# Performance work log

Measured on AMD Instinct MI355X. Metric: run time of the kernel, lower is better.

Reference implementation:

```python
import jax, jax.numpy as jnp
import numpy as np

ORDER = 24
N_POINTS = 524288


def setup_inputs() -> dict:
    key = jax.random.key(0)
    k1, k2 = jax.random.split(key)
    xyz = jax.random.uniform(k1, (N_POINTS, 3), dtype=jnp.float32)
    coeffs = jax.random.normal(k2, (ORDER ** 3,), dtype=jnp.float32) * 0.1
    return {"xyz": xyz, "coeffs": coeffs}


def reference(xyz, coeffs):
    # Faithful to: sum_{i,j,k} c[i,j,k] * sin(2pi i x) * sin(2pi j y) * sin(2pi k z)
    # but with per-axis sin tables computed once (O(order) transcendentals per point)
    # and the triple sum expressed as chained contractions (GEMM-like).
    order = ORDER
    C = coeffs.reshape(order, order, order)  # c[i,j,k]
    n = jnp.arange(order, dtype=xyz.dtype)   # frequencies 0..order-1 (i=0 row is all zeros)
    two_pi = jnp.asarray(2.0 * np.pi, dtype=xyz.dtype)
    S = jnp.sin(two_pi * xyz[:, :, None] * n)  # [N, 3, order]
    Sx, Sy, Sz = S[:, 0, :], S[:, 1, :], S[:, 2, :]  # each [N, order]
    A = jnp.einsum('nk,ijk->nij', Sz, C)   # [N, order, order]
    B = jnp.einsum('nj,nij->ni', Sy, A)    # [N, order]
    return jnp.einsum('ni,ni->n', Sx, B)   # [N]
```

## Files before the change

kernel.cpp:

```cpp
#include <hip/hip_runtime.h>

typedef _Float16 f16x2 __attribute__((ext_vector_type(2)));
typedef _Float16 f16x8 __attribute__((ext_vector_type(8)));
typedef __fp16   fp16v2 __attribute__((ext_vector_type(2)));
typedef float    f32x4 __attribute__((ext_vector_type(4)));
typedef unsigned int u32x4 __attribute__((ext_vector_type(4)));

#define TSTRIDE 17

__device__ __forceinline__ f16x2 pk2(float lo, float hi) {
    fp16v2 p = __builtin_amdgcn_cvt_pkrtz(lo, hi);
    return __builtin_bit_cast(f16x2, p);
}

__global__ __launch_bounds__(256) void prep_B(const float* __restrict__ coeffs,
                                              f16x8* __restrict__ wsB)
{
    int chunk = blockIdx.x * 256 + threadIdx.x;
    int f  = chunk / 48, sl = chunk % 48;
    int s  = f >> 1,  tt = f & 1;
    int gg = sl >> 4, cc = sl & 15;
    int i  = 16 * tt + cc;
    f16x8 v;
    if (i < 24) {
        const float* src = coeffs + i * 576 + s * 24 + gg * 8;
#pragma unroll
        for (int e = 0; e < 8; ++e) v[e] = (_Float16)src[e];
    } else {
#pragma unroll
        for (int e = 0; e < 8; ++e) v[e] = (_Float16)0.f;
    }
    wsB[chunk] = v;
}

__global__ __launch_bounds__(512, 4) void fourier_main(
    const float* __restrict__ xyz,
    const f16x8* __restrict__ wsB,
    float* __restrict__ out)
{
    __shared__ __align__(16) unsigned int Tl[8 * 64 * TSTRIDE];

    const int tid  = threadIdx.x;
    const int wave = tid >> 6;
    const int lane = tid & 63;
    const int g    = lane >> 4;
    const int c    = lane & 15;

    const int p0 = (blockIdx.x * 8 + wave) * 64;

    const float xv = xyz[3 * (p0 + lane)];

    float syp[4], syc[4], c2y[4];
    f16x2 sz2[4][4];
    const float kmask = (g < 3) ? 1.0f : 0.0f;

#pragma unroll
    for (int m = 0; m < 4; ++m) {
        int p = p0 + 16 * m + c;
        float y = xyz[3 * p + 1];
        float z = xyz[3 * p + 2];
        float sy1 = __builtin_amdgcn_sinf(y);
        float cy1 = __builtin_amdgcn_cosf(y);
        syp[m] = 0.f; syc[m] = sy1; c2y[m] = 2.f * cy1;
        float sz1 = __builtin_amdgcn_sinf(z);
        float cz1 = __builtin_amdgcn_cosf(z);
        float wv  = __builtin_amdgcn_fractf((float)(8 * g) * z);
        float sb  = __builtin_amdgcn_sinf(wv) * kmask;
        float cb  = __builtin_amdgcn_cosf(wv);
        float c2z = 2.f * cz1;
        float szf[8];
        szf[0] = sb;
        szf[1] = fmaf(sb, cz1, cb * sz1 * kmask);
#pragma unroll
        for (int e = 2; e < 8; ++e) szf[e] = fmaf(c2z, szf[e - 1], -szf[e - 2]);
#pragma unroll
        for (int q = 0; q < 4; ++q) sz2[m][q] = pk2(szf[2 * q], szf[2 * q + 1]);
    }

    f32x4 acc[4][2] = {};

    const int bslot = (lane < 48) ? lane : 47;
    const f16x8* __restrict__ Bg = wsB;

#pragma unroll
    for (int s = 1; s < 24; ++s) {
        f16x8 b0 = Bg[(2 * s + 0) * 48 + bslot];
        f16x8 b1 = Bg[(2 * s + 1) * 48 + bslot];
#pragma unroll
        for (int m = 0; m < 4; ++m) {
            f16x2 hy2 = pk2(syc[m], syc[m]);
            u32x4 aw;
#pragma unroll
            for (int q = 0; q < 4; ++q) {
                f16x2 pr = hy2 * sz2[m][q];
                aw[q] = __builtin_bit_cast(unsigned int, pr);
            }
            f16x8 a = __builtin_bit_cast(f16x8, aw);
            acc[m][0] = __builtin_amdgcn_mfma_f32_16x16x32_f16(a, b0, acc[m][0], 0, 0, 0);
            acc[m][1] = __builtin_amdgcn_mfma_f32_16x16x32_f16(a, b1, acc[m][1], 0, 0, 0);
            float nxt = fmaf(c2y[m], syc[m], -syp[m]);
            syp[m] = syc[m]; syc[m] = nxt;
        }
    }

    unsigned int* Tw = Tl + wave * (64 * TSTRIDE);
#pragma unroll
    for (int m = 0; m < 4; ++m)
#pragma unroll
        for (int r = 0; r < 4; ++r) {
            int lr = 16 * m + 4 * g + r;
            fp16v2 pk = __builtin_amdgcn_cvt_pkrtz(acc[m][0][r], acc[m][1][r]);
            Tw[lr * TSTRIDE + c] = __builtin_bit_cast(unsigned int, pk);
        }

    asm volatile("s_waitcnt lgkmcnt(0)" ::: "memory");

    {
        int p = p0 + lane;
        float s1  = __builtin_amdgcn_sinf(xv);
        float c1  = __builtin_amdgcn_cosf(xv);
        float w16 = __builtin_amdgcn_fractf(16.f * xv);
        float s16 = __builtin_amdgcn_sinf(w16);
        float c16 = __builtin_amdgcn_cosf(w16);
        const float c2x = 2.f * c1;
        float sA0 = 0.f,  sA1 = s1;
        float sB0 = s16,  sB1 = fmaf(s16, c1, c16 * s1);
        float res = 0.f;
        const unsigned int* Tr = Tw + lane * TSTRIDE;
#pragma unroll
        for (int w = 0; w < 16; ++w) {
            f16x2 h = __builtin_bit_cast(f16x2, Tr[w]);
            res = fmaf(sA0, (float)h[0], res);
            res = fmaf(sB0, (float)h[1], res);
            float nA = fmaf(c2x, sA1, -sA0);
            float nB = fmaf(c2x, sB1, -sB0);
            sA0 = sA1; sA1 = nA;
            sB0 = sB1; sB1 = nB;
        }
        out[p] = res;
    }
}

extern "C" void kernel_launch(void* const* d_in, const int* in_sizes, int n_in,
                              void* d_out, int out_size, void* d_ws, size_t ws_size,
                              hipStream_t stream) {
    const float* xyz    = (const float*)d_in[0];
    const float* coeffs = (const float*)d_in[1];
    float* out = (float*)d_out;
    f16x8* wsB = (f16x8*)d_ws;

    prep_B<<<9, 256, 0, stream>>>(coeffs, wsB);

    const int n = in_sizes[0] / 3;
    const int grid = n / 512;
    fourier_main<<<grid, 512, 0, stream>>>(xyz, wsB, out);
}
```

Before: 31.96 us.

## Switch to 32x32x16 MFMA with register-resident B and dense packed K

Replaces the 16x16x32 MFMA tiling, which padded the z-frequency dimension to 32, with 32x32x16 MFMAs. The (j,k) contraction is packed densely into 35 K-steps of 16, and the y-sine recurrence now advances irregularly across those steps. All B fragments are preloaded into registers once per wave instead of being read from global memory each step. Blocks shrink to 256 threads at launch bound (256,2), and the final x-contraction reads fp32 LDS rows with 16-byte vector loads. The goal is to cut padded MFMA work and global B traffic, at the cost of much higher register pressure and lower occupancy.

```diff
diff --git a/kernel.cpp b/kernel.cpp
--- a/kernel.cpp
+++ b/kernel.cpp
@@ -3,27 +3,30 @@
 typedef _Float16 f16x2 __attribute__((ext_vector_type(2)));
 typedef _Float16 f16x8 __attribute__((ext_vector_type(8)));
 typedef __fp16   fp16v2 __attribute__((ext_vector_type(2)));
-typedef float    f32x4 __attribute__((ext_vector_type(4)));
+typedef float    f32x4  __attribute__((ext_vector_type(4)));
+typedef float    f32x16 __attribute__((ext_vector_type(16)));
 typedef unsigned int u32x4 __attribute__((ext_vector_type(4)));
 
-#define TSTRIDE 17
+#define TROWSTR 28
 
 __device__ __forceinline__ f16x2 pk2(float lo, float hi) {
     fp16v2 p = __builtin_amdgcn_cvt_pkrtz(lo, hi);
     return __builtin_bit_cast(f16x2, p);
+}
+__device__ __forceinline__ unsigned int pkbits(f16x2 a, f16x2 b) {
+    f16x2 r = a * b;
+    return __builtin_bit_cast(unsigned int, r);
 }
 
 __global__ __launch_bounds__(256) void prep_B(const float* __restrict__ coeffs,
                                               f16x8* __restrict__ wsB)
 {
     int chunk = blockIdx.x * 256 + threadIdx.x;
-    int f  = chunk / 48, sl = chunk % 48;
-    int s  = f >> 1,  tt = f & 1;
-    int gg = sl >> 4, cc = sl & 15;
-    int i  = 16 * tt + cc;
+    int s = chunk >> 6, l = chunk & 63;
+    int i = l & 31, h = l >> 5;
     f16x8 v;
     if (i < 24) {
-        const float* src = coeffs + i * 576 + s * 24 + gg * 8;
+        const float* src = coeffs + i * 576 + 16 * s + 8 * h;
 #pragma unroll
         for (int e = 0; e < 8; ++e) v[e] = (_Float16)src[e];
     } else {
@@ -33,109 +36,141 @@
     wsB[chunk] = v;
 }
 
-__global__ __launch_bounds__(512, 4) void fourier_main(
+__global__ __launch_bounds__(256, 2) void fourier_main(
     const float* __restrict__ xyz,
     const f16x8* __restrict__ wsB,
     float* __restrict__ out)
 {
-    __shared__ __align__(16) unsigned int Tl[8 * 64 * TSTRIDE];
+    __shared__ __align__(16) float Tl[4 * 64 * TROWSTR];
 
     const int tid  = threadIdx.x;
     const int wave = tid >> 6;
     const int lane = tid & 63;
-    const int g    = lane >> 4;
-    const int c    = lane & 15;
+    const int h    = lane >> 5;
+    const int mr   = lane & 31;
+    const bool hb  = (h != 0);
 
-    const int p0 = (blockIdx.x * 8 + wave) * 64;
+    const int p0 = (blockIdx.x * 4 + wave) * 64;
 
     const float xv = xyz[3 * (p0 + lane)];
 
-    float syp[4], syc[4], c2y[4];
-    f16x2 sz2[4][4];
-    const float kmask = (g < 3) ? 1.0f : 0.0f;
+    f16x8 bt[36];
+#pragma unroll
+    for (int s = 1; s < 36; ++s) bt[s] = wsB[s * 64 + lane];
+
+    float syp[2], syc[2], c2y[2];
+    f16x2 szR[2][3][4];
 
 #pragma unroll
-    for (int m = 0; m < 4; ++m) {
-        int p = p0 + 16 * m + c;
+    for (int mt = 0; mt < 2; ++mt) {
+        int p = p0 + mt * 32 + mr;
         float y = xyz[3 * p + 1];
         float z = xyz[3 * p + 2];
-        float sy1 = __builtin_amdgcn_sinf(y);
-        float cy1 = __builtin_amdgcn_cosf(y);
-        syp[m] = 0.f; syc[m] = sy1; c2y[m] = 2.f * cy1;
-        float sz1 = __builtin_amdgcn_sinf(z);
-        float cz1 = __builtin_amdgcn_cosf(z);
-        float wv  = __builtin_amdgcn_fractf((float)(8 * g) * z);
-        float sb  = __builtin_amdgcn_sinf(wv) * kmask;
-        float cb  = __builtin_amdgcn_cosf(wv);
-        float c2z = 2.f * cz1;
-        float szf[8];
-        szf[0] = sb;
-        szf[1] = fmaf(sb, cz1, cb * sz1 * kmask);
-#pragma unroll
-        for (int e = 2; e < 8; ++e) szf[e] = fmaf(c2z, szf[e - 1], -szf[e - 2]);
-#pragma unroll
-        for (int q = 0; q < 4; ++q) sz2[m][q] = pk2(szf[2 * q], szf[2 * q + 1]);
-    }
 
-    f32x4 acc[4][2] = {};
+        float s1y = __builtin_amdgcn_sinf(y);
+        float c1y = __builtin_amdgcn_cosf(y);
+        c2y[mt] = 2.f * c1y;
+        syc[mt] = hb ? s1y : 0.f;
+        syp[mt] = hb ? 0.f : -s1y;
 
-    const int bslot = (lane < 48) ? lane : 47;
-    const f16x8* __restrict__ Bg = wsB;
+        float s1 = __builtin_amdgcn_sinf(z);
+        float c1 = __builtin_amdgcn_cosf(z);
+        float w8 = __builtin_amdgcn_fractf(8.f * z);
+        float s8 = __builtin_amdgcn_sinf(w8);
+        float c8 = __builtin_amdgcn_cosf(w8);
+        float s16 = 2.f * s8 * c8;
+        float c16 = fmaf(2.f * c8, c8, -1.f);
+        float c2z = 2.f * c1;
 
 #pragma unroll
-    for (int s = 1; s < 24; ++s) {
-        f16x8 b0 = Bg[(2 * s + 0) * 48 + bslot];
-        f16x8 b1 = Bg[(2 * s + 1) * 48 + bslot];
+        for (int t = 0; t < 3; ++t) {
+            float sk, ck;
+            if (t == 0) { sk = hb ? s8  : 0.f;  ck = hb ? c8  : 1.f;  }
+            if (t == 1) { sk = hb ? s16 : s8;   ck = hb ? c16 : c8;   }
+            if (t == 2) { sk = hb ? 0.f : s16;  ck = hb ? 1.f : c16;  }
+            float v[8];
+            v[0] = sk;
+            v[1] = fmaf(sk, c1, ck * s1);
 #pragma unroll
-        for (int m = 0; m < 4; ++m) {
-            f16x2 hy2 = pk2(syc[m], syc[m]);
-            u32x4 aw;
+            for (int e = 2; e < 8; ++e) v[e] = fmaf(c2z, v[e - 1], -v[e - 2]);
 #pragma unroll
-            for (int q = 0; q < 4; ++q) {
-                f16x2 pr = hy2 * sz2[m][q];
-                aw[q] = __builtin_bit_cast(unsigned int, pr);
-            }
-            f16x8 a = __builtin_bit_cast(f16x8, aw);
-            acc[m][0] = __builtin_amdgcn_mfma_f32_16x16x32_f16(a, b0, acc[m][0], 0, 0, 0);
-            acc[m][1] = __builtin_amdgcn_mfma_f32_16x16x32_f16(a, b1, acc[m][1], 0, 0, 0);
-            float nxt = fmaf(c2y[m], syc[m], -syp[m]);
-            syp[m] = syc[m]; syc[m] = nxt;
+            for (int q = 0; q < 4; ++q) szR[mt][t][q] = pk2(v[2 * q], v[2 * q + 1]);
         }
     }
 
-    unsigned int* Tw = Tl + wave * (64 * TSTRIDE);
+    f32x16 acc0 = {};
+    f32x16 acc1 = {};
+
 #pragma unroll
-    for (int m = 0; m < 4; ++m)
+    for (int s = 1; s < 36; ++s) {
+        const int t = (2 * s) % 3;
+        {
+            f16x2 hy2 = pk2(syc[0], syc[0]);
+            u32x4 aw;
+            aw[0] = pkbits(hy2, szR[0][t][0]);
+            aw[1] = pkbits(hy2, szR[0][t][1]);
+            aw[2] = pkbits(hy2, szR[0][t][2]);
+            aw[3] = pkbits(hy2, szR[0][t][3]);
+            f16x8 a = __builtin_bit_cast(f16x8, aw);
+            acc0 = __builtin_amdgcn_mfma_f32_32x32x16_f16(a, bt[s], acc0, 0, 0, 0);
+        }
+        {
+            f16x2 hy2 = pk2(syc[1], syc[1]);
+            u32x4 aw;
+            aw[0] = pkbits(hy2, szR[1][t][0]);
+            aw[1] = pkbits(hy2, szR[1][t][1]);
+            aw[2] = pkbits(hy2, szR[1][t][2]);
+            aw[3] = pkbits(hy2, szR[1][t][3]);
+            f16x8 a = __builtin_bit_cast(f16x8, aw);
+            acc1 = __builtin_amdgcn_mfma_f32_32x32x16_f16(a, bt[s], acc1, 0, 0, 0);
+        }
+        if (s < 35) {
 #pragma unroll
-        for (int r = 0; r < 4; ++r) {
-            int lr = 16 * m + 4 * g + r;
-            fp16v2 pk = __builtin_amdgcn_cvt_pkrtz(acc[m][0][r], acc[m][1][r]);
-            Tw[lr * TSTRIDE + c] = __builtin_bit_cast(unsigned int, pk);
+            for (int mt = 0; mt < 2; ++mt) {
+                float t1 = fmaf(c2y[mt], syc[mt], -syp[mt]);
+                if ((s % 3) == 2) {
+                    syp[mt] = syc[mt]; syc[mt] = t1;
+                } else {
+                    bool stay = ((s % 3) == 0) ? !hb : hb;
+                    float np = stay ? syp[mt] : syc[mt];
+                    float nc = stay ? syc[mt] : t1;
+                    syp[mt] = np; syc[mt] = nc;
+                }
+            }
         }
+    }
 
+    float* Tw = Tl + wave * (64 * TROWSTR);
+    if (mr < 24) {
+#pragma unroll
+        for (int r = 0; r < 16; ++r) {
+            int row = (r & 3) + 8 * (r >> 2) + 4 * h;
+            Tw[row * TROWSTR + mr]        = acc0[r];
+            Tw[(32 + row) * TROWSTR + mr] = acc1[r];
+        }
+    }
     asm volatile("s_waitcnt lgkmcnt(0)" ::: "memory");
 
     {
         int p = p0 + lane;
         float s1  = __builtin_amdgcn_sinf(xv);
         float c1  = __builtin_amdgcn_cosf(xv);
-        float w16 = __builtin_amdgcn_fractf(16.f * xv);
-        float s16 = __builtin_amdgcn_sinf(w16);
-        float c16 = __builtin_amdgcn_cosf(w16);
         const float c2x = 2.f * c1;
-        float sA0 = 0.f,  sA1 = s1;
-        float sB0 = s16,  sB1 = fmaf(s16, c1, c16 * s1);
-        float res = 0.f;
-        const unsigned int* Tr = Tw + lane * TSTRIDE;
+        const f32x4* T4 = (const f32x4*)(Tw + lane * TROWSTR);
+        f32x4 tv0 = T4[0], tv1 = T4[1], tv2 = T4[2];
+        f32x4 tv3 = T4[3], tv4 = T4[4], tv5 = T4[5];
+        float tv[24];
 #pragma unroll
-        for (int w = 0; w < 16; ++w) {
-            f16x2 h = __builtin_bit_cast(f16x2, Tr[w]);
-            res = fmaf(sA0, (float)h[0], res);
-            res = fmaf(sB0, (float)h[1], res);
-            float nA = fmaf(c2x, sA1, -sA0);
-            float nB = fmaf(c2x, sB1, -sB0);
-            sA0 = sA1; sA1 = nA;
-            sB0 = sB1; sB1 = nB;
+        for (int q = 0; q < 4; ++q) {
+            tv[q]      = tv0[q]; tv[4 + q]  = tv1[q]; tv[8 + q]  = tv2[q];
+            tv[12 + q] = tv3[q]; tv[16 + q] = tv4[q]; tv[20 + q] = tv5[q];
+        }
+        float sp = 0.f, sc = s1, res = 0.f;
+#pragma unroll
+        for (int i = 1; i < 24; ++i) {
+            res = fmaf(sc, tv[i], res);
+            float nx = fmaf(c2x, sc, -sp);
+            sp = sc; sc = nx;
         }
         out[p] = res;
     }
@@ -152,6 +187,6 @@
     prep_B<<<9, 256, 0, stream>>>(coeffs, wsB);
 
     const int n = in_sizes[0] / 3;
-    const int grid = n / 512;
-    fourier_main<<<grid, 512, 0, stream>>>(xyz, wsB, out);
+    const int grid = n / 256;
+    fourier_main<<<grid, 256, 0, stream>>>(xyz, wsB, out);
 }
```

Measured after the change: 31.00 us. 3.0% less time.
